# Optimization experiments

Measured on AMD Instinct MI355X. Metric: run time of the kernel, lower is better.

The kernel has to match this reference:

```python
import jax, jax.numpy as jnp
import numpy as np

B, N, C, H = 4, 4096, 128, 4


def setup_inputs() -> dict:
    key = jax.random.key(0)
    ks = jax.random.split(key, 12)
    def rn(k, shape, s=0.02):
        return jax.random.normal(k, shape, jnp.float32) * s
    return dict(
        x=jax.random.normal(ks[0], (B, N, C), jnp.float32),
        p=jax.random.normal(ks[1], (B, N, 3), jnp.float32),
        fcl1_w=rn(ks[2], (C, C)), fcl1_b=jnp.zeros((C,), jnp.float32),
        # per-head (stacked over leading H axis) TransformerLayer params
        hq_w=rn(ks[3], (H, C, C)), hq_b=jnp.zeros((H, C), jnp.float32),
        hk_w=rn(ks[4], (H, C, C)), hk_b=jnp.zeros((H, C), jnp.float32),
        hv_w=rn(ks[5], (H, C, C)), hv_b=jnp.zeros((H, C), jnp.float32),
        pe1_w=rn(ks[6], (H, C, 3)), pe1_b=jnp.zeros((H, C), jnp.float32),  # Conv1d(3->C, k=1)
        pe2_w=rn(ks[7], (H, C, C)), pe2_b=jnp.zeros((H, C), jnp.float32),  # Conv1d(C->C, k=1)
        mh_w=rn(ks[8], (C, 4 * C)), mh_b=jnp.zeros((C,), jnp.float32),
        fcl2_w=rn(ks[9], (C, C)), fcl2_b=jnp.zeros((C,), jnp.float32),
    )


def reference(x, p, fcl1_w, fcl1_b, hq_w, hq_b, hk_w, hk_b, hv_w, hv_b,
              pe1_w, pe1_b, pe2_w, pe2_b, mh_w, mh_b, fcl2_w, fcl2_b):
    residual = x
    xf = x @ fcl1_w.T + fcl1_b  # fcl1
    scale = 1.0 / jnp.sqrt(jnp.asarray(C, jnp.float32))

    def head(qw, qb, kw, kb, vw, vb, p1w, p1b, p2w, p2b):
        # kernel-size-1 Conv1d == pointwise linear over coords
        pe = jax.nn.relu(jnp.einsum('bnd,cd->bnc', p, p1w) + p1b)
        pe = jnp.einsum('bnc,dc->bnd', pe, p2w) + p2b
        xh = xf + pe
        q = xh @ kw.T + kb  # note: original uses self.key for x_query
        k = xh @ qw.T + qb  # and self.query for x_key (name swap, kept faithful)
        v = xh @ vw.T + vb
        s = jax.nn.softmax(jnp.einsum('bnc,bmc->bnm', q, k) * scale, axis=-1)
        return jnp.einsum('bnm,bmc->bnc', s, v)

    outs = jax.vmap(head)(hq_w, hq_b, hk_w, hk_b, hv_w, hv_b,
                          pe1_w, pe1_b, pe2_w, pe2_b)  # [H,B,N,C]
    cat = jnp.moveaxis(outs, 0, 2).reshape(B, N, H * C)  # concat head1..head4 on last dim
    y = cat @ mh_w.T + mh_b
    y = y @ fcl2_w.T + fcl2_b
    mu = jnp.mean(y, axis=-1, keepdims=True)
    var = jnp.var(y, axis=-1, keepdims=True)
    y = (y - mu) / jnp.sqrt(var + 1e-5)  # torch.layer_norm, no affine
    return (y + residual, p)
```

## Files before the change

kernel.cpp:

```cpp
#include <hip/hip_runtime.h>
#include <hip/hip_bf16.h>

typedef __bf16 bf16;
typedef bf16 bf16x8 __attribute__((ext_vector_type(8)));
typedef float f32x4 __attribute__((ext_vector_type(4)));

static __device__ __forceinline__ f32x4 mfma16(bf16x8 a, bf16x8 b, f32x4 c) {
  return __builtin_amdgcn_mfma_f32_16x16x32_bf16(a, b, c, 0, 0, 0);
}

#define M_TOT 16384
#define CDIM 128
#define N_SEG 18
#define TOTAL_CONV 2511616

__global__ void probe_k(const unsigned short* __restrict__ xr, int* __restrict__ flag) {
  int wild = 0;
#pragma unroll
  for (int i = 0; i < 8; i++) {
    unsigned short w = xr[threadIdx.x * 8 + i];
    int e = (w >> 7) & 0xFF;
    if (e < 110 || e > 134) wild++;
  }
#pragma unroll
  for (int off = 1; off < 64; off <<= 1) wild += __shfl_xor(wild, off);
  if (threadIdx.x == 0) *flag = (wild > 64) ? 1 : 0;
}

struct ConvArgs { const void* src[N_SEG]; };

__global__ __launch_bounds__(256) void convall_k(ConvArgs a, bf16* __restrict__ dst,
                                                 const int* __restrict__ flag) {
  const int ends[N_SEG] = {2097152, 2146304, 2162688, 2162816, 2228352, 2228864,
                           2294400, 2294912, 2360448, 2360960, 2362496, 2363008,
                           2428544, 2429056, 2494592, 2495104, 2511488, 2511616};
  int i = blockIdx.x * 256 + threadIdx.x;
  if (i >= TOTAL_CONV) return;
  int s = 0;
  while (i >= ends[s]) s++;
  int j = i - (s ? ends[s - 1] : 0);
  if (*flag) dst[i] = (bf16)((const float*)a.src[s])[j];
  else       dst[i] = ((const bf16*)a.src[s])[j];
}

__global__ void ppass_k(const void* __restrict__ p, void* __restrict__ out,
                        const int* __restrict__ flag) {
  int i = blockIdx.x * 256 + threadIdx.x;
  if (i >= 49152) return;
  if (*flag) ((float*)out)[2097152 + i] = ((const float*)p)[i];
  else       ((bf16*)out)[2097152 + i]  = ((const bf16*)p)[i];
}

__global__ __launch_bounds__(256) void gemm_k(
    const bf16* __restrict__ A, long aStrZ, int K,
    const bf16* __restrict__ W, long wStrZ,
    const bf16* __restrict__ bias, int bStrZ,
    const bf16* __restrict__ add,
    bf16* __restrict__ out, long outStrZ, int transOut)
{
  const int lane = threadIdx.x & 63;
  const int wave = threadIdx.x >> 6;
  const int quad = lane >> 4;
  const int n15 = lane & 15;
  const bf16* Az = A + (long)blockIdx.z * aStrZ;
  const bf16* Wz = W + (long)blockIdx.z * wStrZ + (long)(blockIdx.y * 64) * K;
  const int r0 = blockIdx.x * 128 + wave * 16;

  f32x4 acc[2][4] = {};
  for (int k0 = 0; k0 < K; k0 += 32) {
    const int ka = k0 + quad * 8;
    bf16x8 a0 = *(const bf16x8*)(Az + (long)(r0 + n15) * K + ka);
    bf16x8 a1 = *(const bf16x8*)(Az + (long)(r0 + 64 + n15) * K + ka);
#pragma unroll
    for (int ct = 0; ct < 4; ct++) {
      bf16x8 wf = *(const bf16x8*)(Wz + (long)(ct * 16 + n15) * K + ka);
      acc[0][ct] = mfma16(a0, wf, acc[0][ct]);
      acc[1][ct] = mfma16(a1, wf, acc[1][ct]);
    }
  }

  bf16* oz = out + (long)blockIdx.z * outStrZ;
#pragma unroll
  for (int s = 0; s < 2; s++) {
    const int rowb = r0 + s * 64 + quad * 4;
#pragma unroll
    for (int ct = 0; ct < 4; ct++) {
      const int col = blockIdx.y * 64 + ct * 16 + n15;
      const float bval = (float)bias[(long)blockIdx.z * bStrZ + col];
#pragma unroll
      for (int r = 0; r < 4; r++) {
        float v = acc[s][ct][r] + bval;
        if (add) v += (float)add[(long)(rowb + r) * CDIM + col];
        if (transOut) oz[(long)col * M_TOT + rowb + r] = (bf16)v;
        else          oz[(long)(rowb + r) * CDIM + col] = (bf16)v;
      }
    }
  }
}

__global__ __launch_bounds__(256) void pe1_k(
    const bf16* __restrict__ p, const bf16* __restrict__ w,
    const bf16* __restrict__ bias, bf16* __restrict__ pe)
{
  const int h = blockIdx.y;
  const int m = blockIdx.x * 2 + (threadIdx.x >> 7);
  const int c = threadIdx.x & 127;
  const float p0 = (float)p[m * 3 + 0];
  const float p1 = (float)p[m * 3 + 1];
  const float p2 = (float)p[m * 3 + 2];
  const bf16* wh = w + ((long)h * 128 + c) * 3;
  float v = p0 * (float)wh[0] + p1 * (float)wh[1] + p2 * (float)wh[2]
          + (float)bias[h * 128 + c];
  pe[((long)h * 16384 + m) * 128 + c] = (bf16)fmaxf(v, 0.f);
}

__global__ __launch_bounds__(256) void qkv_k(
    const bf16* __restrict__ A,
    const bf16* __restrict__ Wq, const bf16* __restrict__ Bq,
    const bf16* __restrict__ Wk, const bf16* __restrict__ Bk,
    const bf16* __restrict__ Wv, const bf16* __restrict__ Bv,
    bf16* __restrict__ qo, bf16* __restrict__ ko, bf16* __restrict__ vo)
{
  const int lane = threadIdx.x & 63;
  const int wave = threadIdx.x >> 6;
  const int quad = lane >> 4;
  const int n15 = lane & 15;
  const int h = blockIdx.z;
  const bf16* Az = A + (long)h * 2097152;
  const long wBase = (long)h * 16384 + (long)(blockIdx.y * 64) * 128;
  const int r0 = blockIdx.x * 128 + wave * 16;

  f32x4 acc[3][2][4] = {};
  for (int k0 = 0; k0 < 128; k0 += 32) {
    const int ka = k0 + quad * 8;
    bf16x8 a0 = *(const bf16x8*)(Az + (long)(r0 + n15) * 128 + ka);
    bf16x8 a1 = *(const bf16x8*)(Az + (long)(r0 + 64 + n15) * 128 + ka);
#pragma unroll
    for (int ct = 0; ct < 4; ct++) {
      const long wrow = wBase + (long)(ct * 16 + n15) * 128 + ka;
      bf16x8 wq = *(const bf16x8*)(Wq + wrow);
      bf16x8 wk = *(const bf16x8*)(Wk + wrow);
      bf16x8 wv = *(const bf16x8*)(Wv + wrow);
      acc[0][0][ct] = mfma16(a0, wq, acc[0][0][ct]);
      acc[0][1][ct] = mfma16(a1, wq, acc[0][1][ct]);
      acc[1][0][ct] = mfma16(a0, wk, acc[1][0][ct]);
      acc[1][1][ct] = mfma16(a1, wk, acc[1][1][ct]);
      acc[2][0][ct] = mfma16(a0, wv, acc[2][0][ct]);
      acc[2][1][ct] = mfma16(a1, wv, acc[2][1][ct]);
    }
  }

  bf16* qz = qo + (long)h * 2097152;
  bf16* kz = ko + (long)h * 2097152;
  bf16* vz = vo + (long)h * 2097152;
#pragma unroll
  for (int s = 0; s < 2; s++) {
    const int rowb = r0 + s * 64 + quad * 4;
#pragma unroll
    for (int ct = 0; ct < 4; ct++) {
      const int col = blockIdx.y * 64 + ct * 16 + n15;
      const float bq = (float)Bq[h * 128 + col];
      const float bk = (float)Bk[h * 128 + col];
      const float bv = (float)Bv[h * 128 + col];
#pragma unroll
      for (int r = 0; r < 4; r++) {
        qz[(long)(rowb + r) * 128 + col] = (bf16)(acc[0][s][ct][r] + bq);
        kz[(long)(rowb + r) * 128 + col] = (bf16)(acc[1][s][ct][r] + bk);
        vz[(long)col * M_TOT + rowb + r] = (bf16)(acc[2][s][ct][r] + bv);
      }
    }
  }
}

__global__ __launch_bounds__(256, 2) void attn_k(
    const bf16* __restrict__ Q, const bf16* __restrict__ Kg,
    const bf16* __restrict__ vT, bf16* __restrict__ cat)
{
  const int lane = threadIdx.x & 63;
  const int wave = threadIdx.x >> 6;
  const int quad = lane >> 4;
  const int n15 = lane & 15;
  const int b = blockIdx.y, h = blockIdx.z;
  const long qkBase = ((long)h * 4 + b) * 4096 * 128;
  const long vBase = (long)h * (128L * 16384) + (long)b * 4096;
  const int wrow = blockIdx.x * 128 + wave * 32;

  __shared__ bf16 Kt[64 * 128];
  __shared__ bf16 Vt[128 * 64];
  __shared__ bf16 Pt[4][16][72];

  const float scale = 0.08838834764831845f;
  bf16x8 qf[2][4];
#pragma unroll
  for (int g = 0; g < 2; g++)
#pragma unroll
    for (int kk = 0; kk < 4; kk++) {
      bf16x8 t = *(const bf16x8*)(Q + qkBase + (long)(wrow + g * 16 + n15) * 128 + kk * 32 + quad * 8);
#pragma unroll
      for (int j = 0; j < 8; j++) t[j] = (bf16)((float)t[j] * scale);
      qf[g][kk] = t;
    }

  f32x4 Om[2][8] = {};
  float l_part[2][4] = {};

  for (int kv0 = 0; kv0 < 4096; kv0 += 64) {
    __syncthreads();
    {
      const int rr = threadIdx.x >> 4;
      const int ch = threadIdx.x & 15;
#pragma unroll
      for (int i = 0; i < 4; i++) {
        const int row = rr + i * 16;
        *(bf16x8*)&Kt[row * 128 + ((ch ^ rr) * 8)] =
            *(const bf16x8*)(Kg + qkBase + (long)(kv0 + row) * 128 + ch * 8);
      }
      const int vc = threadIdx.x >> 3;
      const int vch = threadIdx.x & 7;
#pragma unroll
      for (int i = 0; i < 4; i++) {
        const int c = vc + i * 32;
        *(bf16x8*)&Vt[c * 64 + ((vch ^ (c & 7)) * 8)] =
            *(const bf16x8*)(vT + vBase + (long)c * 16384 + kv0 + vch * 8);
      }
    }
    __syncthreads();

    f32x4 S[2][4] = {};
#pragma unroll
    for (int kk = 0; kk < 4; kk++) {
#pragma unroll
      for (int ct = 0; ct < 4; ct++) {
        bf16x8 kf = *(const bf16x8*)&Kt[(ct * 16 + n15) * 128 + (((kk * 4 + quad) ^ n15) * 8)];
        S[0][ct] = mfma16(qf[0][kk], kf, S[0][ct]);
        S[1][ct] = mfma16(qf[1][kk], kf, S[1][ct]);
      }
    }

    bf16x8 pf[2][2];
#pragma unroll
    for (int g = 0; g < 2; g++) {
#pragma unroll
      for (int ct = 0; ct < 4; ct++)
#pragma unroll
        for (int r = 0; r < 4; r++) {
          float e = __expf(S[g][ct][r]);
          l_part[g][r] += e;
          Pt[wave][quad * 4 + r][ct * 16 + n15] = (bf16)e;
        }
      pf[g][0] = *(const bf16x8*)&Pt[wave][n15][quad * 8];
      pf[g][1] = *(const bf16x8*)&Pt[wave][n15][32 + quad * 8];
    }

#pragma unroll
    for (int kk = 0; kk < 2; kk++) {
      bf16x8 vf[8];
#pragma unroll
      for (int ct = 0; ct < 8; ct++) {
        const int c = ct * 16 + n15;
        vf[ct] = *(const bf16x8*)&Vt[c * 64 + (((kk * 4 + quad) ^ (c & 7)) * 8)];
      }
#pragma unroll
      for (int g = 0; g < 2; g++)
#pragma unroll
        for (int ct = 0; ct < 8; ct++)
          Om[g][ct] = mfma16(pf[g][kk], vf[ct], Om[g][ct]);
    }
  }

#pragma unroll
  for (int g = 0; g < 2; g++) {
    float inv[4];
#pragma unroll
    for (int r = 0; r < 4; r++) {
      float s = l_part[g][r];
#pragma unroll
      for (int off = 1; off < 16; off <<= 1) s += __shfl_xor(s, off);
      inv[r] = 1.f / s;
    }
    const long ob = ((long)b * 4096 + wrow + g * 16 + quad * 4) * 512 + h * 128;
#pragma unroll
    for (int ct = 0; ct < 8; ct++)
#pragma unroll
      for (int r = 0; r < 4; r++)
        cat[ob + (long)r * 512 + ct * 16 + n15] = (bf16)(Om[g][ct][r] * inv[r]);
  }
}

__global__ __launch_bounds__(256) void tail_k(
    const bf16* __restrict__ cat,
    const bf16* __restrict__ mhw, const bf16* __restrict__ mhb,
    const bf16* __restrict__ f2w, const bf16* __restrict__ f2b,
    const void* __restrict__ xraw, void* __restrict__ outraw,
    const int* __restrict__ flag)
{
  const int lane = threadIdx.x & 63;
  const int wave = threadIdx.x >> 6;
  const int quad = lane >> 4;
  const int n15 = lane & 15;
  const int r0 = blockIdx.x * 64 + wave * 16;
  __shared__ bf16 y1t[64][136];

  f32x4 acc[8] = {};
  for (int k0 = 0; k0 < 512; k0 += 32) {
    const int ka = k0 + quad * 8;
    bf16x8 a0 = *(const bf16x8*)(cat + (long)(r0 + n15) * 512 + ka);
#pragma unroll
    for (int ct = 0; ct < 8; ct++) {
      bf16x8 wf = *(const bf16x8*)(mhw + (long)(ct * 16 + n15) * 512 + ka);
      acc[ct] = mfma16(a0, wf, acc[ct]);
    }
  }
#pragma unroll
  for (int ct = 0; ct < 8; ct++) {
    const float bv = (float)mhb[ct * 16 + n15];
#pragma unroll
    for (int r = 0; r < 4; r++)
      y1t[wave * 16 + quad * 4 + r][ct * 16 + n15] = (bf16)(acc[ct][r] + bv);
  }
  __syncthreads();

  f32x4 acc2[8] = {};
  for (int k0 = 0; k0 < 128; k0 += 32) {
    const int ka = k0 + quad * 8;
    bf16x8 a0 = *(const bf16x8*)&y1t[wave * 16 + n15][ka];
#pragma unroll
    for (int ct = 0; ct < 8; ct++) {
      bf16x8 wf = *(const bf16x8*)(f2w + (long)(ct * 16 + n15) * 128 + ka);
      acc2[ct] = mfma16(a0, wf, acc2[ct]);
    }
  }

  float s1[4] = {}, s2[4] = {};
#pragma unroll
  for (int ct = 0; ct < 8; ct++) {
    const float bv = (float)f2b[ct * 16 + n15];
#pragma unroll
    for (int r = 0; r < 4; r++) {
      const float v = acc2[ct][r] + bv;
      acc2[ct][r] = v;
      s1[r] += v;
      s2[r] += v * v;
    }
  }
  float mu[4], inv[4];
#pragma unroll
  for (int r = 0; r < 4; r++) {
    float a = s1[r], b2 = s2[r];
#pragma unroll
    for (int off = 1; off < 16; off <<= 1) {
      a += __shfl_xor(a, off);
      b2 += __shfl_xor(b2, off);
    }
    mu[r] = a * (1.f / 128.f);
    const float var = fmaxf(b2 * (1.f / 128.f) - mu[r] * mu[r], 0.f);
    inv[r] = rsqrtf(var + 1e-5f);
  }

  const int isF32 = *flag;
#pragma unroll
  for (int ct = 0; ct < 8; ct++)
#pragma unroll
    for (int r = 0; r < 4; r++) {
      const long idx = (long)(r0 + quad * 4 + r) * 128 + ct * 16 + n15;
      const float resid = isF32 ? ((const float*)xraw)[idx]
                                : (float)((const bf16*)xraw)[idx];
      const float v = (acc2[ct][r] - mu[r]) * inv[r] + resid;
      if (isF32) ((float*)outraw)[idx] = v;
      else       ((bf16*)outraw)[idx] = (bf16)v;
    }
}

extern "C" void kernel_launch(void* const* d_in, const int* in_sizes, int n_in,
                              void* d_out, int out_size, void* d_ws, size_t ws_size,
                              hipStream_t stream)
{
  bf16* ws  = (bf16*)d_ws;
  bf16* xf  = ws;
  bf16* pe  = ws + 2097152;
  bf16* xh  = ws + 10485760;
  bf16* kb  = ws + 18874368;
  bf16* vt  = ws + 27262976;
  bf16* cat = ws + 35651584;
  const long AR = 44040192;
  int* flag = (int*)(ws + 46551808);
  bf16* q   = pe;

  static const int counts[N_SEG] = {2097152, 49152, 16384, 128, 65536, 512, 65536, 512,
                                    65536, 512, 1536, 512, 65536, 512, 65536, 512, 16384, 128};
  long offs[N_SEG]; long o = AR;
  for (int i = 0; i < N_SEG; i++) { offs[i] = o; o += counts[i]; }
  bf16* xc    = ws + offs[0];
  bf16* pc    = ws + offs[1];
  bf16* f1w   = ws + offs[2];
  bf16* f1b   = ws + offs[3];
  bf16* hqw   = ws + offs[4];
  bf16* hqb   = ws + offs[5];
  bf16* hkw   = ws + offs[6];
  bf16* hkb   = ws + offs[7];
  bf16* hvw   = ws + offs[8];
  bf16* hvb   = ws + offs[9];
  bf16* pe1w  = ws + offs[10];
  bf16* pe1b  = ws + offs[11];
  bf16* pe2w  = ws + offs[12];
  bf16* pe2b  = ws + offs[13];
  bf16* mhw   = ws + offs[14];
  bf16* mhb   = ws + offs[15];
  bf16* f2w   = ws + offs[16];
  bf16* f2b   = ws + offs[17];

  probe_k<<<dim3(1), dim3(64), 0, stream>>>((const unsigned short*)d_in[0], flag);
  ConvArgs ca;
  for (int i = 0; i < N_SEG; i++) ca.src[i] = d_in[i];
  convall_k<<<dim3((TOTAL_CONV + 255) / 256), dim3(256), 0, stream>>>(ca, ws + AR, flag);

  dim3 blk(256);
  gemm_k<<<dim3(128, 2, 1), blk, 0, stream>>>(xc, 0, 128, f1w, 0, f1b, 0, nullptr, xf, 0, 0);
  pe1_k<<<dim3(8192, 4, 1), blk, 0, stream>>>(pc, pe1w, pe1b, pe);
  gemm_k<<<dim3(128, 2, 4), blk, 0, stream>>>(pe, 2097152L, 128, pe2w, 16384L, pe2b, 128, xf, xh, 2097152L, 0);
  qkv_k<<<dim3(128, 2, 4), blk, 0, stream>>>(xh, hkw, hkb, hqw, hqb, hvw, hvb, q, kb, vt);
  attn_k<<<dim3(32, 4, 4), blk, 0, stream>>>(q, kb, vt, cat);
  tail_k<<<dim3(256), blk, 0, stream>>>(cat, mhw, mhb, f2w, f2b, d_in[0], d_out, flag);
  ppass_k<<<dim3(192), dim3(256), 0, stream>>>(d_in[1], d_out, flag);
}
```

Before: 367.4 us.

## Fuse pre-attention GEMMs into one kernel, widen attention KV tile, merge p copy

Replaces the fcl1 GEMM, pe1, pe2 GEMM and QKV kernels with a single pre_k kernel per (row block, head). It keeps xf and the positional encoding in shared memory, so the xf, pe and xh intermediates no longer go through global memory. The attention kernel now stages 128 KV rows per iteration with a 16-way XOR swizzle, which halves the number of barriers and loop iterations but doubles shared memory use and may reduce occupancy. The p passthrough copy is folded into the conversion kernel, and a __syncthreads in the tail kernel is removed. That barrier removal looks safe only if each wave reads back just the y1t rows it wrote itself.

```diff
diff --git a/kernel.cpp b/kernel.cpp
--- a/kernel.cpp
+++ b/kernel.cpp
@@ -30,12 +30,20 @@
 struct ConvArgs { const void* src[N_SEG]; };
 
 __global__ __launch_bounds__(256) void convall_k(ConvArgs a, bf16* __restrict__ dst,
+                                                 void* __restrict__ outp,
                                                  const int* __restrict__ flag) {
   const int ends[N_SEG] = {2097152, 2146304, 2162688, 2162816, 2228352, 2228864,
                            2294400, 2294912, 2360448, 2360960, 2362496, 2363008,
                            2428544, 2429056, 2494592, 2495104, 2511488, 2511616};
   int i = blockIdx.x * 256 + threadIdx.x;
-  if (i >= TOTAL_CONV) return;
+  if (i >= TOTAL_CONV) {
+    int j = i - TOTAL_CONV;
+    if (j < 49152) {
+      if (*flag) ((float*)outp)[2097152 + j] = ((const float*)a.src[1])[j];
+      else       ((bf16*)outp)[2097152 + j]  = ((const bf16*)a.src[1])[j];
+    }
+    return;
+  }
   int s = 0;
   while (i >= ends[s]) s++;
   int j = i - (s ? ends[s - 1] : 0);
@@ -43,79 +51,11 @@
   else       dst[i] = ((const bf16*)a.src[s])[j];
 }
 
-__global__ void ppass_k(const void* __restrict__ p, void* __restrict__ out,
-                        const int* __restrict__ flag) {
-  int i = blockIdx.x * 256 + threadIdx.x;
-  if (i >= 49152) return;
-  if (*flag) ((float*)out)[2097152 + i] = ((const float*)p)[i];
-  else       ((bf16*)out)[2097152 + i]  = ((const bf16*)p)[i];
-}
-
-__global__ __launch_bounds__(256) void gemm_k(
-    const bf16* __restrict__ A, long aStrZ, int K,
-    const bf16* __restrict__ W, long wStrZ,
-    const bf16* __restrict__ bias, int bStrZ,
-    const bf16* __restrict__ add,
-    bf16* __restrict__ out, long outStrZ, int transOut)
-{
-  const int lane = threadIdx.x & 63;
-  const int wave = threadIdx.x >> 6;
-  const int quad = lane >> 4;
-  const int n15 = lane & 15;
-  const bf16* Az = A + (long)blockIdx.z * aStrZ;
-  const bf16* Wz = W + (long)blockIdx.z * wStrZ + (long)(blockIdx.y * 64) * K;
-  const int r0 = blockIdx.x * 128 + wave * 16;
-
-  f32x4 acc[2][4] = {};
-  for (int k0 = 0; k0 < K; k0 += 32) {
-    const int ka = k0 + quad * 8;
-    bf16x8 a0 = *(const bf16x8*)(Az + (long)(r0 + n15) * K + ka);
-    bf16x8 a1 = *(const bf16x8*)(Az + (long)(r0 + 64 + n15) * K + ka);
-#pragma unroll
-    for (int ct = 0; ct < 4; ct++) {
-      bf16x8 wf = *(const bf16x8*)(Wz + (long)(ct * 16 + n15) * K + ka);
-      acc[0][ct] = mfma16(a0, wf, acc[0][ct]);
-      acc[1][ct] = mfma16(a1, wf, acc[1][ct]);
-    }
-  }
-
-  bf16* oz = out + (long)blockIdx.z * outStrZ;
-#pragma unroll
-  for (int s = 0; s < 2; s++) {
-    const int rowb = r0 + s * 64 + quad * 4;
-#pragma unroll
-    for (int ct = 0; ct < 4; ct++) {
-      const int col = blockIdx.y * 64 + ct * 16 + n15;
-      const float bval = (float)bias[(long)blockIdx.z * bStrZ + col];
-#pragma unroll
-      for (int r = 0; r < 4; r++) {
-        float v = acc[s][ct][r] + bval;
-        if (add) v += (float)add[(long)(rowb + r) * CDIM + col];
-        if (transOut) oz[(long)col * M_TOT + rowb + r] = (bf16)v;
-        else          oz[(long)(rowb + r) * CDIM + col] = (bf16)v;
-      }
-    }
-  }
-}
-
-__global__ __launch_bounds__(256) void pe1_k(
-    const bf16* __restrict__ p, const bf16* __restrict__ w,
-    const bf16* __restrict__ bias, bf16* __restrict__ pe)
-{
-  const int h = blockIdx.y;
-  const int m = blockIdx.x * 2 + (threadIdx.x >> 7);
-  const int c = threadIdx.x & 127;
-  const float p0 = (float)p[m * 3 + 0];
-  const float p1 = (float)p[m * 3 + 1];
-  const float p2 = (float)p[m * 3 + 2];
-  const bf16* wh = w + ((long)h * 128 + c) * 3;
-  float v = p0 * (float)wh[0] + p1 * (float)wh[1] + p2 * (float)wh[2]
-          + (float)bias[h * 128 + c];
-  pe[((long)h * 16384 + m) * 128 + c] = (bf16)fmaxf(v, 0.f);
-}
-
-__global__ __launch_bounds__(256) void qkv_k(
-    const bf16* __restrict__ A,
+__global__ __launch_bounds__(256, 2) void pre_k(
+    const bf16* __restrict__ x, const bf16* __restrict__ p,
+    const bf16* __restrict__ f1w, const bf16* __restrict__ f1b,
+    const bf16* __restrict__ pe1w, const bf16* __restrict__ pe1b,
+    const bf16* __restrict__ pe2w, const bf16* __restrict__ pe2b,
     const bf16* __restrict__ Wq, const bf16* __restrict__ Bq,
     const bf16* __restrict__ Wk, const bf16* __restrict__ Bk,
     const bf16* __restrict__ Wv, const bf16* __restrict__ Bv,
@@ -125,49 +65,138 @@
   const int wave = threadIdx.x >> 6;
   const int quad = lane >> 4;
   const int n15 = lane & 15;
-  const int h = blockIdx.z;
-  const bf16* Az = A + (long)h * 2097152;
-  const long wBase = (long)h * 16384 + (long)(blockIdx.y * 64) * 128;
-  const int r0 = blockIdx.x * 128 + wave * 16;
-
-  f32x4 acc[3][2][4] = {};
-  for (int k0 = 0; k0 < 128; k0 += 32) {
-    const int ka = k0 + quad * 8;
-    bf16x8 a0 = *(const bf16x8*)(Az + (long)(r0 + n15) * 128 + ka);
-    bf16x8 a1 = *(const bf16x8*)(Az + (long)(r0 + 64 + n15) * 128 + ka);
-#pragma unroll
-    for (int ct = 0; ct < 4; ct++) {
-      const long wrow = wBase + (long)(ct * 16 + n15) * 128 + ka;
-      bf16x8 wq = *(const bf16x8*)(Wq + wrow);
-      bf16x8 wk = *(const bf16x8*)(Wk + wrow);
-      bf16x8 wv = *(const bf16x8*)(Wv + wrow);
-      acc[0][0][ct] = mfma16(a0, wq, acc[0][0][ct]);
-      acc[0][1][ct] = mfma16(a1, wq, acc[0][1][ct]);
-      acc[1][0][ct] = mfma16(a0, wk, acc[1][0][ct]);
-      acc[1][1][ct] = mfma16(a1, wk, acc[1][1][ct]);
-      acc[2][0][ct] = mfma16(a0, wv, acc[2][0][ct]);
-      acc[2][1][ct] = mfma16(a1, wv, acc[2][1][ct]);
-    }
-  }
-
-  bf16* qz = qo + (long)h * 2097152;
-  bf16* kz = ko + (long)h * 2097152;
-  bf16* vz = vo + (long)h * 2097152;
-#pragma unroll
-  for (int s = 0; s < 2; s++) {
-    const int rowb = r0 + s * 64 + quad * 4;
-#pragma unroll
-    for (int ct = 0; ct < 4; ct++) {
-      const int col = blockIdx.y * 64 + ct * 16 + n15;
-      const float bq = (float)Bq[h * 128 + col];
-      const float bk = (float)Bk[h * 128 + col];
-      const float bv = (float)Bv[h * 128 + col];
-#pragma unroll
-      for (int r = 0; r < 4; r++) {
-        qz[(long)(rowb + r) * 128 + col] = (bf16)(acc[0][s][ct][r] + bq);
-        kz[(long)(rowb + r) * 128 + col] = (bf16)(acc[1][s][ct][r] + bk);
-        vz[(long)col * M_TOT + rowb + r] = (bf16)(acc[2][s][ct][r] + bv);
-      }
+  const int h = blockIdx.y;
+  const int r0 = blockIdx.x * 128;
+  const int wr = wave * 32;
+
+  __shared__ bf16 xft[128][136];
+  __shared__ bf16 pet[128][136];
+  __shared__ bf16 pst[4][32][4];
+  __shared__ bf16 wst[4][128][4];
+
+  {
+    f32x4 acc[2][8] = {};
+#pragma unroll
+    for (int kk = 0; kk < 4; kk++) {
+      const int ka = kk * 32 + quad * 8;
+      bf16x8 a0 = *(const bf16x8*)(x + (long)(r0 + wr + n15) * 128 + ka);
+      bf16x8 a1 = *(const bf16x8*)(x + (long)(r0 + wr + 16 + n15) * 128 + ka);
+#pragma unroll
+      for (int ct = 0; ct < 8; ct++) {
+        bf16x8 wf = *(const bf16x8*)(f1w + (long)(ct * 16 + n15) * 128 + ka);
+        acc[0][ct] = mfma16(a0, wf, acc[0][ct]);
+        acc[1][ct] = mfma16(a1, wf, acc[1][ct]);
+      }
+    }
+#pragma unroll
+    for (int g = 0; g < 2; g++)
+#pragma unroll
+      for (int ct = 0; ct < 8; ct++) {
+        const int col = ct * 16 + n15;
+        const float bv = (float)f1b[col];
+#pragma unroll
+        for (int r = 0; r < 4; r++)
+          xft[wr + g * 16 + quad * 4 + r][col] = (bf16)(acc[g][ct][r] + bv);
+      }
+  }
+
+  if (lane < 32) {
+    const bf16* pr = p + (long)(r0 + wr + lane) * 3;
+    pst[wave][lane][0] = pr[0]; pst[wave][lane][1] = pr[1]; pst[wave][lane][2] = pr[2];
+  }
+  for (int i = lane; i < 128; i += 64) {
+    const bf16* wrp = pe1w + ((long)h * 128 + i) * 3;
+    wst[wave][i][0] = wrp[0]; wst[wave][i][1] = wrp[1]; wst[wave][i][2] = wrp[2];
+  }
+#pragma unroll
+  for (int cc = 0; cc < 2; cc++) {
+    const int c = cc * 64 + lane;
+    const float w0 = (float)wst[wave][c][0];
+    const float w1 = (float)wst[wave][c][1];
+    const float w2 = (float)wst[wave][c][2];
+    const float bb = (float)pe1b[h * 128 + c];
+    for (int rr = 0; rr < 32; rr++) {
+      const float p0 = (float)pst[wave][rr][0];
+      const float p1 = (float)pst[wave][rr][1];
+      const float p2 = (float)pst[wave][rr][2];
+      pet[wr + rr][c] = (bf16)fmaxf(p0 * w0 + p1 * w1 + p2 * w2 + bb, 0.f);
+    }
+  }
+
+  {
+    f32x4 acc[2][8] = {};
+#pragma unroll
+    for (int kk = 0; kk < 4; kk++) {
+      const int ka = kk * 32 + quad * 8;
+      bf16x8 a0 = *(const bf16x8*)&pet[wr + n15][ka];
+      bf16x8 a1 = *(const bf16x8*)&pet[wr + 16 + n15][ka];
+#pragma unroll
+      for (int ct = 0; ct < 8; ct++) {
+        bf16x8 wf = *(const bf16x8*)(pe2w + (long)h * 16384 + (long)(ct * 16 + n15) * 128 + ka);
+        acc[0][ct] = mfma16(a0, wf, acc[0][ct]);
+        acc[1][ct] = mfma16(a1, wf, acc[1][ct]);
+      }
+    }
+#pragma unroll
+    for (int g = 0; g < 2; g++)
+#pragma unroll
+      for (int ct = 0; ct < 8; ct++) {
+        const int col = ct * 16 + n15;
+        const float bv = (float)pe2b[h * 128 + col];
+#pragma unroll
+        for (int r = 0; r < 4; r++) {
+          const int rl = wr + g * 16 + quad * 4 + r;
+          xft[rl][col] = (bf16)(acc[g][ct][r] + bv + (float)xft[rl][col]);
+        }
+      }
+  }
+
+  bf16x8 af[2][4];
+#pragma unroll
+  for (int g = 0; g < 2; g++)
+#pragma unroll
+    for (int kk = 0; kk < 4; kk++)
+      af[g][kk] = *(const bf16x8*)&xft[wr + g * 16 + n15][kk * 32 + quad * 8];
+
+  const bf16* Ws[3] = {Wq, Wk, Wv};
+  const bf16* Bs[3] = {Bq, Bk, Bv};
+#pragma unroll
+  for (int m = 0; m < 3; m++) {
+    f32x4 acc[2][8] = {};
+#pragma unroll
+    for (int kk = 0; kk < 4; kk++) {
+      const int ka = kk * 32 + quad * 8;
+#pragma unroll
+      for (int ct = 0; ct < 8; ct++) {
+        bf16x8 wf = *(const bf16x8*)(Ws[m] + (long)h * 16384 + (long)(ct * 16 + n15) * 128 + ka);
+        acc[0][ct] = mfma16(af[0][kk], wf, acc[0][ct]);
+        acc[1][ct] = mfma16(af[1][kk], wf, acc[1][ct]);
+      }
+    }
+    if (m < 2) {
+      bf16* oz = (m == 0 ? qo : ko) + (long)h * 2097152;
+#pragma unroll
+      for (int g = 0; g < 2; g++)
+#pragma unroll
+        for (int ct = 0; ct < 8; ct++) {
+          const int col = ct * 16 + n15;
+          const float bv = (float)Bs[m][h * 128 + col];
+#pragma unroll
+          for (int r = 0; r < 4; r++)
+            oz[(long)(r0 + wr + g * 16 + quad * 4 + r) * 128 + col] = (bf16)(acc[g][ct][r] + bv);
+        }
+    } else {
+      bf16* vz = vo + (long)h * (128L * 16384);
+#pragma unroll
+      for (int g = 0; g < 2; g++)
+#pragma unroll
+        for (int ct = 0; ct < 8; ct++) {
+          const int col = ct * 16 + n15;
+          const float bv = (float)Bs[2][h * 128 + col];
+#pragma unroll
+          for (int r = 0; r < 4; r++)
+            vz[(long)col * 16384 + (r0 + wr + g * 16 + quad * 4 + r)] = (bf16)(acc[g][ct][r] + bv);
+        }
     }
   }
 }
@@ -185,9 +214,9 @@
   const long vBase = (long)h * (128L * 16384) + (long)b * 4096;
   const int wrow = blockIdx.x * 128 + wave * 32;
 
-  __shared__ bf16 Kt[64 * 128];
-  __shared__ bf16 Vt[128 * 64];
-  __shared__ bf16 Pt[4][16][72];
+  __shared__ bf16 Kt[128 * 128];
+  __shared__ bf16 Vt[128 * 128];
+  __shared__ bf16 Pt[4][16 * 128];
 
   const float scale = 0.08838834764831845f;
   bf16x8 qf[2][4];
@@ -204,61 +233,63 @@
   f32x4 Om[2][8] = {};
   float l_part[2][4] = {};
 
-  for (int kv0 = 0; kv0 < 4096; kv0 += 64) {
+  for (int kv0 = 0; kv0 < 4096; kv0 += 128) {
     __syncthreads();
     {
       const int rr = threadIdx.x >> 4;
       const int ch = threadIdx.x & 15;
 #pragma unroll
-      for (int i = 0; i < 4; i++) {
+      for (int i = 0; i < 8; i++) {
         const int row = rr + i * 16;
-        *(bf16x8*)&Kt[row * 128 + ((ch ^ rr) * 8)] =
+        *(bf16x8*)&Kt[row * 128 + ((ch ^ (row & 15)) * 8)] =
             *(const bf16x8*)(Kg + qkBase + (long)(kv0 + row) * 128 + ch * 8);
       }
-      const int vc = threadIdx.x >> 3;
-      const int vch = threadIdx.x & 7;
-#pragma unroll
-      for (int i = 0; i < 4; i++) {
-        const int c = vc + i * 32;
-        *(bf16x8*)&Vt[c * 64 + ((vch ^ (c & 7)) * 8)] =
-            *(const bf16x8*)(vT + vBase + (long)c * 16384 + kv0 + vch * 8);
+#pragma unroll
+      for (int i = 0; i < 8; i++) {
+        const int c = rr + i * 16;
+        *(bf16x8*)&Vt[c * 128 + ((ch ^ (c & 15)) * 8)] =
+            *(const bf16x8*)(vT + vBase + (long)c * 16384 + kv0 + ch * 8);
       }
     }
     __syncthreads();
 
-    f32x4 S[2][4] = {};
-#pragma unroll
-    for (int kk = 0; kk < 4; kk++) {
-#pragma unroll
-      for (int ct = 0; ct < 4; ct++) {
-        bf16x8 kf = *(const bf16x8*)&Kt[(ct * 16 + n15) * 128 + (((kk * 4 + quad) ^ n15) * 8)];
+    f32x4 S[2][8] = {};
+#pragma unroll
+    for (int kk = 0; kk < 4; kk++) {
+#pragma unroll
+      for (int ct = 0; ct < 8; ct++) {
+        const int row = ct * 16 + n15;
+        bf16x8 kf = *(const bf16x8*)&Kt[row * 128 + (((kk * 4 + quad) ^ (row & 15)) * 8)];
         S[0][ct] = mfma16(qf[0][kk], kf, S[0][ct]);
         S[1][ct] = mfma16(qf[1][kk], kf, S[1][ct]);
       }
     }
 
-    bf16x8 pf[2][2];
+    bf16x8 pf[2][4];
 #pragma unroll
     for (int g = 0; g < 2; g++) {
 #pragma unroll
-      for (int ct = 0; ct < 4; ct++)
+      for (int ct = 0; ct < 8; ct++)
 #pragma unroll
         for (int r = 0; r < 4; r++) {
           float e = __expf(S[g][ct][r]);
           l_part[g][r] += e;
-          Pt[wave][quad * 4 + r][ct * 16 + n15] = (bf16)e;
+          const int row = quad * 4 + r;
+          const int kv = ct * 16 + n15;
+          Pt[wave][row * 128 + (((kv >> 3) ^ row) * 8) + (kv & 7)] = (bf16)e;
         }
-      pf[g][0] = *(const bf16x8*)&Pt[wave][n15][quad * 8];
-      pf[g][1] = *(const bf16x8*)&Pt[wave][n15][32 + quad * 8];
-    }
-
-#pragma unroll
-    for (int kk = 0; kk < 2; kk++) {
+#pragma unroll
+      for (int kk = 0; kk < 4; kk++)
+        pf[g][kk] = *(const bf16x8*)&Pt[wave][n15 * 128 + (((kk * 4 + quad) ^ n15) * 8)];
+    }
+
+#pragma unroll
+    for (int kk = 0; kk < 4; kk++) {
       bf16x8 vf[8];
 #pragma unroll
       for (int ct = 0; ct < 8; ct++) {
         const int c = ct * 16 + n15;
-        vf[ct] = *(const bf16x8*)&Vt[c * 64 + (((kk * 4 + quad) ^ (c & 7)) * 8)];
+        vf[ct] = *(const bf16x8*)&Vt[c * 128 + (((kk * 4 + quad) ^ (c & 15)) * 8)];
       }
 #pragma unroll
       for (int g = 0; g < 2; g++)
@@ -318,7 +349,6 @@
     for (int r = 0; r < 4; r++)
       y1t[wave * 16 + quad * 4 + r][ct * 16 + n15] = (bf16)(acc[ct][r] + bv);
   }
-  __syncthreads();
 
   f32x4 acc2[8] = {};
   for (int k0 = 0; k0 < 128; k0 += 32) {
@@ -376,15 +406,12 @@
                               hipStream_t stream)
 {
   bf16* ws  = (bf16*)d_ws;
-  bf16* xf  = ws;
-  bf16* pe  = ws + 2097152;
-  bf16* xh  = ws + 10485760;
+  bf16* q   = ws + 2097152;
   bf16* kb  = ws + 18874368;
   bf16* vt  = ws + 27262976;
   bf16* cat = ws + 35651584;
   const long AR = 44040192;
   int* flag = (int*)(ws + 46551808);
-  bf16* q   = pe;
 
   static const int counts[N_SEG] = {2097152, 49152, 16384, 128, 65536, 512, 65536, 512,
                                     65536, 512, 1536, 512, 65536, 512, 65536, 512, 16384, 128};
@@ -412,14 +439,11 @@
   probe_k<<<dim3(1), dim3(64), 0, stream>>>((const unsigned short*)d_in[0], flag);
   ConvArgs ca;
   for (int i = 0; i < N_SEG; i++) ca.src[i] = d_in[i];
-  convall_k<<<dim3((TOTAL_CONV + 255) / 256), dim3(256), 0, stream>>>(ca, ws + AR, flag);
+  convall_k<<<dim3((TOTAL_CONV + 49152 + 255) / 256), dim3(256), 0, stream>>>(ca, ws + AR, d_out, flag);
 
   dim3 blk(256);
-  gemm_k<<<dim3(128, 2, 1), blk, 0, stream>>>(xc, 0, 128, f1w, 0, f1b, 0, nullptr, xf, 0, 0);
-  pe1_k<<<dim3(8192, 4, 1), blk, 0, stream>>>(pc, pe1w, pe1b, pe);
-  gemm_k<<<dim3(128, 2, 4), blk, 0, stream>>>(pe, 2097152L, 128, pe2w, 16384L, pe2b, 128, xf, xh, 2097152L, 0);
-  qkv_k<<<dim3(128, 2, 4), blk, 0, stream>>>(xh, hkw, hkb, hqw, hqb, hvw, hvb, q, kb, vt);
+  pre_k<<<dim3(128, 4), blk, 0, stream>>>(xc, pc, f1w, f1b, pe1w, pe1b, pe2w, pe2b,
+                                          hkw, hkb, hqw, hqb, hvw, hvb, q, kb, vt);
   attn_k<<<dim3(32, 4, 4), blk, 0, stream>>>(q, kb, vt, cat);
   tail_k<<<dim3(256), blk, 0, stream>>>(cat, mhw, mhb, f2w, f2b, d_in[0], d_out, flag);
-  ppass_k<<<dim3(192), dim3(256), 0, stream>>>(d_in[1], d_out, flag);
-}
+}
```

Measured after the change: 400.1 us. 8.9% more time.
